# Kernel optimization log

Measured on AMD Instinct MI355X. Metric: run time of the kernel, lower is better.

Reference implementation:

```python
import jax, jax.numpy as jnp
import numpy as np

N, B, FIN, FOUT = 4096, 16, 128, 128
DENSITY = 0.01


def setup_inputs() -> dict:
    key = jax.random.key(0)
    k1, k2, k3, k4 = jax.random.split(key, 4)
    # sparse binary adjacency (static pattern), stored dense for the reference
    adj = (jax.random.uniform(k1, (N, N)) < DENSITY).astype(jnp.float32)
    x = jax.random.normal(k2, (B, N, FIN), dtype=jnp.float32)
    W = jax.random.normal(k3, (FOUT, FIN), dtype=jnp.float32) * (1.0 / np.sqrt(FIN))
    b = jax.random.normal(k4, (FOUT,), dtype=jnp.float32) * 0.01
    return {"adj": adj, "x": x, "W": W, "b": b}


def _normalized_adj(adj):
    # A_hat = D^{-1/2} (A + I) D^{-1/2}, degrees from column sums (dim=0 in torch)
    a_self = adj + jnp.eye(adj.shape[0], dtype=adj.dtype)
    dinv = jax.lax.rsqrt(jnp.sum(a_self, axis=0))
    return dinv[:, None] * a_self * dinv[None, :]


def reference(adj, x, W, b):
    a_norm = _normalized_adj(adj)
    # SpMM aggregation over nodes: (N,N) x (B,N,F) -> (B,N,F)
    agg = jnp.einsum('nm,bmf->bnf', a_norm, x)
    # dense linear transform: fc(agg)
    return jnp.einsum('bnf,of->bno', agg, W) + b
```

## Files before the change

### kernel.cpp

```cpp
#include <hip/hip_runtime.h>


#define NN 4096
#define FD 128
#define NB 16
#define CAP 96
#define CPAD 104

typedef float     f32x4 __attribute__((ext_vector_type(4)));
typedef _Float16  f16x4 __attribute__((ext_vector_type(4)));
typedef _Float16  f16x8 __attribute__((ext_vector_type(8)));
typedef int       i32x2 __attribute__((ext_vector_type(2)));
typedef int       i32x4 __attribute__((ext_vector_type(4)));

#define XP 136

__device__ __forceinline__ float fmamix_lo(float acc, int pk, float w) {
    asm("v_fma_mix_f32 %0, %1, %2, %0 op_sel:[0,0,0] op_sel_hi:[1,0,0]"
        : "+v"(acc) : "v"(pk), "v"(w));
    return acc;
}
__device__ __forceinline__ float fmamix_hi(float acc, int pk, float w) {
    asm("v_fma_mix_f32 %0, %1, %2, %0 op_sel:[1,0,0] op_sel_hi:[1,0,0]"
        : "+v"(acc) : "v"(pk), "v"(w));
    return acc;
}

__global__ __launch_bounds__(256) void k_xform(const float* __restrict__ x,
                                               const float* __restrict__ W,
                                               _Float16* __restrict__ y) {
    __shared__ _Float16 sW[FD][XP];
    const int t = threadIdx.x;

    #pragma unroll
    for (int i = 0; i < 8; ++i) {
        const int id = t + i * 256;
        const int o = id >> 4, f8 = (id & 15) * 8;
        const f32x4 a = *(const f32x4*)&W[(size_t)o * FD + f8];
        const f32x4 b = *(const f32x4*)&W[(size_t)o * FD + f8 + 4];
        f16x8 h;
        h[0]=(_Float16)a.x; h[1]=(_Float16)a.y; h[2]=(_Float16)a.z; h[3]=(_Float16)a.w;
        h[4]=(_Float16)b.x; h[5]=(_Float16)b.y; h[6]=(_Float16)b.z; h[7]=(_Float16)b.w;
        *(f16x8*)&sW[o][f8] = h;
    }
    __syncthreads();

    const int w = t >> 6, lane = t & 63;
    const int lrow = lane & 15, koct = (lane >> 4) * 8;
    const size_t rbase = (size_t)blockIdx.x * 64;
    const float* xr = x + (rbase + w * 16 + lrow) * FD;
    f32x4 acc[8] = {};
    #pragma unroll
    for (int kc = 0; kc < 4; ++kc) {
        const int ko = kc * 32 + koct;
        const f32x4 a0 = *(const f32x4*)&xr[ko];
        const f32x4 a1 = *(const f32x4*)&xr[ko + 4];
        f16x8 xx;
        xx[0]=(_Float16)a0.x; xx[1]=(_Float16)a0.y; xx[2]=(_Float16)a0.z; xx[3]=(_Float16)a0.w;
        xx[4]=(_Float16)a1.x; xx[5]=(_Float16)a1.y; xx[6]=(_Float16)a1.z; xx[7]=(_Float16)a1.w;
        #pragma unroll
        for (int ot = 0; ot < 8; ++ot) {
            const f16x8 ww = *(const f16x8*)&sW[ot * 16 + lrow][ko];
            acc[ot] = __builtin_amdgcn_mfma_f32_16x16x32_f16(ww, xx, acc[ot], 0, 0, 0);
        }
    }
    const size_t row = rbase + w * 16 + (lane & 15);
    #pragma unroll
    for (int ot = 0; ot < 8; ++ot) {
        f16x4 h;
        h[0] = (_Float16)acc[ot][0];
        h[1] = (_Float16)acc[ot][1];
        h[2] = (_Float16)acc[ot][2];
        h[3] = (_Float16)acc[ot][3];
        *(f16x4*)&y[row * FD + ot * 16 + (lane >> 4) * 4] = h;
    }
}

__global__ __launch_bounds__(256) void k_build(const float* __restrict__ A,
                                               float* __restrict__ deg,
                                               int* __restrict__ cnt,
                                               unsigned short* __restrict__ csr) {
    __shared__ int sWsum[4];
    const int n = blockIdx.x, t = threadIdx.x;
    const int w = t >> 6, lane = t & 63;
    const float* row = A + (size_t)n * NN + t * 16;
    float r[16];
    *(f32x4*)&r[0]  = ((const f32x4*)row)[0];
    *(f32x4*)&r[4]  = ((const f32x4*)row)[1];
    *(f32x4*)&r[8]  = ((const f32x4*)row)[2];
    *(f32x4*)&r[12] = ((const f32x4*)row)[3];

    int c = 0;
    #pragma unroll
    for (int j = 0; j < 16; ++j) c += (r[j] != 0.0f) ? 1 : 0;

    int s = c;
    #pragma unroll
    for (int off = 1; off < 64; off <<= 1) {
        const int u = __shfl(s, lane - off);
        s += (lane >= off) ? u : 0;
    }
    if (lane == 63) sWsum[w] = s;
    __syncthreads();
    int wbase = 0;
    #pragma unroll
    for (int j = 0; j < 4; ++j) wbase += (j < w) ? sWsum[j] : 0;

    int pos = wbase + s - c;
    #pragma unroll
    for (int j = 0; j < 16; ++j) {
        if (r[j] != 0.0f) {
            const int m = t * 16 + j;
            if (pos < CAP) csr[(size_t)n * CAP + pos] = (unsigned short)m;
            ++pos;
            atomicAdd(&deg[m], 1.0f);
        }
    }
    if (t == 255) {
        const int tot = wbase + s;
        cnt[n] = tot < CAP ? tot : CAP;
    }
}

__global__ __launch_bounds__(256) void k_agg2(const _Float16* __restrict__ y,
                                              const int* __restrict__ cnt,
                                              const unsigned short* __restrict__ csr,
                                              const float* __restrict__ deg,
                                              const float* __restrict__ bias,
                                              float* __restrict__ out) {
    __shared__ int sL[4][CPAD * 2];
    const int t = threadIdx.x, w = t >> 6, lane = t & 63;
    const int bid = blockIdx.x;
    const int xcd = bid & 7;
    const int b0  = 2 * xcd;
    const int n   = (bid >> 3) * 4 + w;
    const int c = cnt[n];
    const int totPad = (c + 1 + 3) & ~3;

    for (int k = lane; k < CPAD; k += 64) {
        int m; float wv;
        if (k < c)       { m = csr[(size_t)n * CAP + k]; wv = rsqrtf(1.0f + deg[m]); }
        else if (k == c) { m = n; wv = rsqrtf(1.0f + deg[n]); }
        else             { m = n; wv = 0.0f; }
        sL[w][2 * k]     = m << 8;
        sL[w][2 * k + 1] = __float_as_int(wv);
    }
    __syncthreads();

    const int rq = lane >> 4;
    const int fo = (lane & 15) * 16;
    const char* yb0 = (const char*)y + (size_t)b0 * (NN * FD * 2);
    const char* yb1 = yb0 + (size_t)(NN * FD * 2);

    float acc0[8] = {}, acc1[8] = {};
    i32x2 e = *(const i32x2*)&sL[w][2 * rq];
    unsigned voff = (unsigned)(e.x + fo);
    i32x4 pA = *(const i32x4*)(yb0 + voff);
    i32x4 pB = *(const i32x4*)(yb1 + voff);
    float wt = __int_as_float(e.y);
    for (int k = rq + 4; k < totPad; k += 4) {
        const i32x2 e2 = *(const i32x2*)&sL[w][2 * k];
        const unsigned v2 = (unsigned)(e2.x + fo);
        const i32x4 nA = *(const i32x4*)(yb0 + v2);
        const i32x4 nB = *(const i32x4*)(yb1 + v2);
        const float wt2 = __int_as_float(e2.y);
        #pragma unroll
        for (int j = 0; j < 4; ++j) {
            acc0[2*j]   = fmamix_lo(acc0[2*j],   pA[j], wt);
            acc0[2*j+1] = fmamix_hi(acc0[2*j+1], pA[j], wt);
            acc1[2*j]   = fmamix_lo(acc1[2*j],   pB[j], wt);
            acc1[2*j+1] = fmamix_hi(acc1[2*j+1], pB[j], wt);
        }
        pA = nA; pB = nB; wt = wt2;
    }
    #pragma unroll
    for (int j = 0; j < 4; ++j) {
        acc0[2*j]   = fmamix_lo(acc0[2*j],   pA[j], wt);
        acc0[2*j+1] = fmamix_hi(acc0[2*j+1], pA[j], wt);
        acc1[2*j]   = fmamix_lo(acc1[2*j],   pB[j], wt);
        acc1[2*j+1] = fmamix_hi(acc1[2*j+1], pB[j], wt);
    }

    #pragma unroll
    for (int j = 0; j < 8; ++j) {
        acc0[j] += __shfl_xor(acc0[j], 16);
        acc0[j] += __shfl_xor(acc0[j], 32);
        acc1[j] += __shfl_xor(acc1[j], 16);
        acc1[j] += __shfl_xor(acc1[j], 32);
    }

    if (lane < 32) {
        const float dn = rsqrtf(1.0f + deg[n]);
        const int h = lane >> 4;
        const int f0 = (lane & 15) * 8 + h * 4;
        const f32x4 bb = *(const f32x4*)(bias + f0);
        f32x4 o0, o1;
        o0.x = acc0[h * 4 + 0] * dn + bb.x;
        o0.y = acc0[h * 4 + 1] * dn + bb.y;
        o0.z = acc0[h * 4 + 2] * dn + bb.z;
        o0.w = acc0[h * 4 + 3] * dn + bb.w;
        o1.x = acc1[h * 4 + 0] * dn + bb.x;
        o1.y = acc1[h * 4 + 1] * dn + bb.y;
        o1.z = acc1[h * 4 + 2] * dn + bb.z;
        o1.w = acc1[h * 4 + 3] * dn + bb.w;
        f32x4* d0 = (f32x4*)(out + ((size_t)b0 * NN + n) * FD + f0);
        f32x4* d1 = (f32x4*)(out + ((size_t)(b0 + 1) * NN + n) * FD + f0);
        __builtin_nontemporal_store(o0, d0);
        __builtin_nontemporal_store(o1, d1);
    }
}

extern "C" void kernel_launch(void* const* d_in, const int* in_sizes, int n_in,
                              void* d_out, int out_size, void* d_ws, size_t ws_size,
                              hipStream_t stream) {
    const float* A    = (const float*)d_in[0];
    const float* x    = (const float*)d_in[1];
    const float* W    = (const float*)d_in[2];
    const float* bias = (const float*)d_in[3];
    float* out = (float*)d_out;

    float*          deg  = (float*)d_ws;
    int*            cnt  = (int*)((char*)d_ws + 2 * NN * 4);
    unsigned short* csr  = (unsigned short*)(cnt + NN);
    _Float16*       y    = (_Float16*)((char*)d_ws + (3 * NN * 4 + (size_t)NN * CAP * 2));

    hipMemsetAsync(deg, 0, NN * sizeof(float), stream);
    k_xform<<<(NB * NN) / 64, 256, 0, stream>>>(x, W, y);
    k_build<<<NN, 256, 0, stream>>>(A, deg, cnt, csr);
    k_agg2 <<<(NN / 4) * (NB / 2), 256, 0, stream>>>(y, cnt, csr, deg, bias, out);
}
```

Baseline: 81.29 us.

## Merge transform and CSR build kernels into one launch, read W from global

The x·W transform and the adjacency CSR build become one kernel that splits work by block index: the first 1024 blocks run the MFMA transform and the remaining 4096 build the CSR. The transform no longer stages W as fp16 in shared memory. It loads and converts W from global (L2-cached) per tile, which drops the LDS staging and the barrier. The aggregation loop drops its manual software prefetch in favour of a plain loop with unroll 2. This saves one launch and lets the two independent phases overlap, at the cost of redundant W loads and conversions in every block and possibly less latency hiding in the gather loop.

```diff
diff --git a/kernel.cpp b/kernel.cpp
--- a/kernel.cpp
+++ b/kernel.cpp
@@ -6,6 +6,7 @@
 #define NB 16
 #define CAP 96
 #define CPAD 104
+#define XB 1024
 
 typedef float     f32x4 __attribute__((ext_vector_type(4)));
 typedef _Float16  f16x4 __attribute__((ext_vector_type(4)));
@@ -13,8 +14,6 @@
 typedef int       i32x2 __attribute__((ext_vector_type(2)));
 typedef int       i32x4 __attribute__((ext_vector_type(4)));
 
-#define XP 136
-
 __device__ __forceinline__ float fmamix_lo(float acc, int pk, float w) {
     asm("v_fma_mix_f32 %0, %1, %2, %0 op_sel:[0,0,0] op_sel_hi:[1,0,0]"
         : "+v"(acc) : "v"(pk), "v"(w));
@@ -26,63 +25,55 @@
     return acc;
 }
 
-__global__ __launch_bounds__(256) void k_xform(const float* __restrict__ x,
-                                               const float* __restrict__ W,
-                                               _Float16* __restrict__ y) {
-    __shared__ _Float16 sW[FD][XP];
+__global__ __launch_bounds__(256) void k_bx(const float* __restrict__ A,
+                                            float* __restrict__ deg,
+                                            int* __restrict__ cnt,
+                                            unsigned short* __restrict__ csr,
+                                            const float* __restrict__ x,
+                                            const float* __restrict__ W,
+                                            _Float16* __restrict__ y) {
+    __shared__ int sWsum[4];
     const int t = threadIdx.x;
-
-    #pragma unroll
-    for (int i = 0; i < 8; ++i) {
-        const int id = t + i * 256;
-        const int o = id >> 4, f8 = (id & 15) * 8;
-        const f32x4 a = *(const f32x4*)&W[(size_t)o * FD + f8];
-        const f32x4 b = *(const f32x4*)&W[(size_t)o * FD + f8 + 4];
-        f16x8 h;
-        h[0]=(_Float16)a.x; h[1]=(_Float16)a.y; h[2]=(_Float16)a.z; h[3]=(_Float16)a.w;
-        h[4]=(_Float16)b.x; h[5]=(_Float16)b.y; h[6]=(_Float16)b.z; h[7]=(_Float16)b.w;
-        *(f16x8*)&sW[o][f8] = h;
-    }
-    __syncthreads();
-
     const int w = t >> 6, lane = t & 63;
-    const int lrow = lane & 15, koct = (lane >> 4) * 8;
-    const size_t rbase = (size_t)blockIdx.x * 64;
-    const float* xr = x + (rbase + w * 16 + lrow) * FD;
-    f32x4 acc[8] = {};
-    #pragma unroll
-    for (int kc = 0; kc < 4; ++kc) {
-        const int ko = kc * 32 + koct;
-        const f32x4 a0 = *(const f32x4*)&xr[ko];
-        const f32x4 a1 = *(const f32x4*)&xr[ko + 4];
-        f16x8 xx;
-        xx[0]=(_Float16)a0.x; xx[1]=(_Float16)a0.y; xx[2]=(_Float16)a0.z; xx[3]=(_Float16)a0.w;
-        xx[4]=(_Float16)a1.x; xx[5]=(_Float16)a1.y; xx[6]=(_Float16)a1.z; xx[7]=(_Float16)a1.w;
+
+    if (blockIdx.x < XB) {
+        const int lrow = lane & 15, koct = (lane >> 4) * 8;
+        const size_t rbase = (size_t)blockIdx.x * 64;
+        const float* xr = x + (rbase + w * 16 + lrow) * FD;
+        f32x4 acc[8] = {};
+        #pragma unroll
+        for (int kc = 0; kc < 4; ++kc) {
+            const int ko = kc * 32 + koct;
+            const f32x4 a0 = *(const f32x4*)&xr[ko];
+            const f32x4 a1 = *(const f32x4*)&xr[ko + 4];
+            f16x8 xx;
+            xx[0]=(_Float16)a0.x; xx[1]=(_Float16)a0.y; xx[2]=(_Float16)a0.z; xx[3]=(_Float16)a0.w;
+            xx[4]=(_Float16)a1.x; xx[5]=(_Float16)a1.y; xx[6]=(_Float16)a1.z; xx[7]=(_Float16)a1.w;
+            #pragma unroll
+            for (int ot = 0; ot < 8; ++ot) {
+                const float* wr = W + (size_t)(ot * 16 + lrow) * FD + ko;
+                const f32x4 w0 = *(const f32x4*)&wr[0];
+                const f32x4 w1 = *(const f32x4*)&wr[4];
+                f16x8 ww;
+                ww[0]=(_Float16)w0.x; ww[1]=(_Float16)w0.y; ww[2]=(_Float16)w0.z; ww[3]=(_Float16)w0.w;
+                ww[4]=(_Float16)w1.x; ww[5]=(_Float16)w1.y; ww[6]=(_Float16)w1.z; ww[7]=(_Float16)w1.w;
+                acc[ot] = __builtin_amdgcn_mfma_f32_16x16x32_f16(ww, xx, acc[ot], 0, 0, 0);
+            }
+        }
+        const size_t row = rbase + w * 16 + lrow;
         #pragma unroll
         for (int ot = 0; ot < 8; ++ot) {
-            const f16x8 ww = *(const f16x8*)&sW[ot * 16 + lrow][ko];
-            acc[ot] = __builtin_amdgcn_mfma_f32_16x16x32_f16(ww, xx, acc[ot], 0, 0, 0);
-        }
-    }
-    const size_t row = rbase + w * 16 + (lane & 15);
-    #pragma unroll
-    for (int ot = 0; ot < 8; ++ot) {
-        f16x4 h;
-        h[0] = (_Float16)acc[ot][0];
-        h[1] = (_Float16)acc[ot][1];
-        h[2] = (_Float16)acc[ot][2];
-        h[3] = (_Float16)acc[ot][3];
-        *(f16x4*)&y[row * FD + ot * 16 + (lane >> 4) * 4] = h;
-    }
-}
-
-__global__ __launch_bounds__(256) void k_build(const float* __restrict__ A,
-                                               float* __restrict__ deg,
-                                               int* __restrict__ cnt,
-                                               unsigned short* __restrict__ csr) {
-    __shared__ int sWsum[4];
-    const int n = blockIdx.x, t = threadIdx.x;
-    const int w = t >> 6, lane = t & 63;
+            f16x4 h;
+            h[0] = (_Float16)acc[ot][0];
+            h[1] = (_Float16)acc[ot][1];
+            h[2] = (_Float16)acc[ot][2];
+            h[3] = (_Float16)acc[ot][3];
+            *(f16x4*)&y[row * FD + ot * 16 + (lane >> 4) * 4] = h;
+        }
+        return;
+    }
+
+    const int n = blockIdx.x - XB;
     const float* row = A + (size_t)n * NN + t * 16;
     float r[16];
     *(f32x4*)&r[0]  = ((const f32x4*)row)[0];
@@ -153,17 +144,13 @@
     const char* yb1 = yb0 + (size_t)(NN * FD * 2);
 
     float acc0[8] = {}, acc1[8] = {};
-    i32x2 e = *(const i32x2*)&sL[w][2 * rq];
-    unsigned voff = (unsigned)(e.x + fo);
-    i32x4 pA = *(const i32x4*)(yb0 + voff);
-    i32x4 pB = *(const i32x4*)(yb1 + voff);
-    float wt = __int_as_float(e.y);
-    for (int k = rq + 4; k < totPad; k += 4) {
-        const i32x2 e2 = *(const i32x2*)&sL[w][2 * k];
-        const unsigned v2 = (unsigned)(e2.x + fo);
-        const i32x4 nA = *(const i32x4*)(yb0 + v2);
-        const i32x4 nB = *(const i32x4*)(yb1 + v2);
-        const float wt2 = __int_as_float(e2.y);
+    #pragma unroll 2
+    for (int k = rq; k < totPad; k += 4) {
+        const i32x2 e = *(const i32x2*)&sL[w][2 * k];
+        const unsigned v = (unsigned)(e.x + fo);
+        const i32x4 pA = *(const i32x4*)(yb0 + v);
+        const i32x4 pB = *(const i32x4*)(yb1 + v);
+        const float wt = __int_as_float(e.y);
         #pragma unroll
         for (int j = 0; j < 4; ++j) {
             acc0[2*j]   = fmamix_lo(acc0[2*j],   pA[j], wt);
@@ -171,14 +158,6 @@
             acc1[2*j]   = fmamix_lo(acc1[2*j],   pB[j], wt);
             acc1[2*j+1] = fmamix_hi(acc1[2*j+1], pB[j], wt);
         }
-        pA = nA; pB = nB; wt = wt2;
-    }
-    #pragma unroll
-    for (int j = 0; j < 4; ++j) {
-        acc0[2*j]   = fmamix_lo(acc0[2*j],   pA[j], wt);
-        acc0[2*j+1] = fmamix_hi(acc0[2*j+1], pA[j], wt);
-        acc1[2*j]   = fmamix_lo(acc1[2*j],   pB[j], wt);
-        acc1[2*j+1] = fmamix_hi(acc1[2*j+1], pB[j], wt);
     }
 
     #pragma unroll
@@ -225,7 +204,6 @@
     _Float16*       y    = (_Float16*)((char*)d_ws + (3 * NN * 4 + (size_t)NN * CAP * 2));
 
     hipMemsetAsync(deg, 0, NN * sizeof(float), stream);
-    k_xform<<<(NB * NN) / 64, 256, 0, stream>>>(x, W, y);
-    k_build<<<NN, 256, 0, stream>>>(A, deg, cnt, csr);
-    k_agg2 <<<(NN / 4) * (NB / 2), 256, 0, stream>>>(y, cnt, csr, deg, bias, out);
-}
+    k_bx  <<<XB + NN, 256, 0, stream>>>(A, deg, cnt, csr, x, W, y);
+    k_agg2<<<(NN / 4) * (NB / 2), 256, 0, stream>>>(y, cnt, csr, deg, bias, out);
+}
```

Result: slower. 94.33 us (+16.0%).
